# Performance work log

Hardware: AMD Instinct MI355X
Metric: run time of the kernel (lower is better)

## Reference

```python
import math
import jax, jax.numpy as jnp
import numpy as np

D_MODEL = 256
NUM_FEATURES = 512  # 2 * d_model (module default)
BATCH, SEQ = 4, 4096
EPS = 1e-6
INPUT_SCALE = 0.25  # keeps exp(xW/sqrt(d) - ||x||^2/2) numerically meaningful


def _make_projection(key):
    # Orthogonal random features: ceil(M/d)=2 QR blocks, then sqrt(|gauss|) row scaling.
    k1, k2, k3 = jax.random.split(key, 3)
    q1, _ = jnp.linalg.qr(jax.random.normal(k1, (D_MODEL, D_MODEL), jnp.float32))
    q2, _ = jnp.linalg.qr(jax.random.normal(k2, (D_MODEL, D_MODEL), jnp.float32))
    proj = jnp.concatenate([q1, q2], axis=1)[:, :NUM_FEATURES]  # (d, M)
    scaling = jnp.sqrt(jnp.abs(jax.random.normal(k3, (D_MODEL, 1), jnp.float32)))
    return proj * scaling


def setup_inputs() -> dict:
    key = jax.random.key(0)
    kq, kk, kv, kp = jax.random.split(key, 4)
    shape = (BATCH, SEQ, D_MODEL)
    return {
        "query": jax.random.normal(kq, shape, jnp.float32) * INPUT_SCALE,
        "key": jax.random.normal(kk, shape, jnp.float32) * INPUT_SCALE,
        "value": jax.random.normal(kv, shape, jnp.float32) * INPUT_SCALE,
        "projection": _make_projection(kp),  # (d_model, num_features) buffer
    }


def _phi(x, projection):
    # phi(x) = exp(xW/sqrt(d) - ||x||^2/2) / sqrt(M)
    d = x.shape[-1]
    m = projection.shape[-1]
    proj = jnp.matmul(x, projection) / math.sqrt(d)  # (B, L, M)
    sq = 0.5 * jnp.sum(x * x, axis=-1, keepdims=True)  # (B, L, 1)
    return jnp.exp(proj - sq) / math.sqrt(m)


def reference(query, key, value, projection):
    qp = _phi(query, projection)  # (B, L, M)
    kp = _phi(key, projection)    # (B, L, M)
    B, L, M = qp.shape
    D = value.shape[-1]

    # Causal linear attention: running KV-state scan, O(B*M*D) state
    # (same math as cumsum of k' (outer) v, without materializing (B,L,M,D)).
    def step(carry, inp):
        kv_state, k_state = carry  # (B,M,D), (B,M)
        q_t, k_t, v_t = inp        # (B,M), (B,M), (B,D)
        kv_state = kv_state + k_t[:, :, None] * v_t[:, None, :]
        k_state = k_state + k_t
        num = jnp.einsum('bm,bmd->bd', q_t, kv_state)
        den = jnp.einsum('bm,bm->b', q_t, k_state)[:, None] + EPS
        return (kv_state, k_state), num / den

    init = (jnp.zeros((B, M, D), qp.dtype), jnp.zeros((B, M), qp.dtype))
    xs = (jnp.swapaxes(qp, 0, 1), jnp.swapaxes(kp, 0, 1), jnp.swapaxes(value, 0, 1))
    _, out = jax.lax.scan(step, init, xs)  # (L, B, D)
    return jnp.swapaxes(out, 0, 1)  # (B, L, D)
```

## Files before the change

### kernel.cpp

```cpp
#include <hip/hip_runtime.h>

#define B_ 4
#define L_ 4096
#define D_ 256
#define M_ 512
#define C_ 256
#define NC_ 16
#define NG_ (B_*NC_)
#define EPS_ 1e-6f
#define RSQRT_D_ 0.0625f
#define RSQRT_M_ 0.044194173824159216f

typedef __attribute__((ext_vector_type(8))) short short8;
typedef __attribute__((ext_vector_type(4))) short short4v;
typedef __attribute__((ext_vector_type(4))) float floatx4;

__device__ __forceinline__ short f2b(float f) {
  union { float f; unsigned u; } c; c.f = f;
  unsigned r = c.u + 0x7fffu + ((c.u >> 16) & 1u);
  return (short)(r >> 16);
}
__device__ __forceinline__ float b2f(short s) {
  union { unsigned u; float f; } c; c.u = ((unsigned)(unsigned short)s) << 16;
  return c.f;
}

#define OFF_SB   0u
#define OFF_WT   16777216u
#define OFF_QP   17039360u
#define OFF_KP   33816576u
#define OFF_KPT  50593792u
#define OFF_VT   67371008u
#define OFF_AM   75759616u
#define OFF_PB   84148224u
#define OFF_ZP   100925440u

__device__ __forceinline__ void mfma_tile_gemm(
    const short* __restrict__ Ag, int lda,
    const short* __restrict__ Bg, int ldb,
    int K, short* sA, short* sB, floatx4 acc[4][4])
{
  const int tid  = threadIdx.x;
  const int lane = tid & 63;
  const int wave = tid >> 6;
  const int wm = wave >> 1, wn = wave & 1;
  const int q = lane >> 4, ml = lane & 15;

  short8 pa[4], pb[4];
  #pragma unroll
  for (int it = 0; it < 4; ++it) {
    int ci = tid + 256 * it;
    int m = ci >> 3, k8 = ci & 7;
    pa[it] = *(const short8*)(Ag + (size_t)m * lda + k8 * 8);
    pb[it] = *(const short8*)(Bg + (size_t)m * ldb + k8 * 8);
  }
  for (int k0 = 0; k0 < K; k0 += 64) {
    #pragma unroll
    for (int it = 0; it < 4; ++it) {
      int ci = tid + 256 * it;
      int m = ci >> 3, k8 = ci & 7;
      int dst = (k8 >> 2) * 512 + (m >> 4) * 64 + (k8 & 3) * 16 + ((m & 15) ^ k8);
      *(short8*)(sA + dst * 8) = pa[it];
      *(short8*)(sB + dst * 8) = pb[it];
    }
    if (k0 + 64 < K) {
      #pragma unroll
      for (int it = 0; it < 4; ++it) {
        int ci = tid + 256 * it;
        int m = ci >> 3, k8 = ci & 7;
        pa[it] = *(const short8*)(Ag + (size_t)m * lda + k0 + 64 + k8 * 8);
        pb[it] = *(const short8*)(Bg + (size_t)m * ldb + k0 + 64 + k8 * 8);
      }
    }
    __syncthreads();
    #pragma unroll
    for (int ks = 0; ks < 2; ++ks) {
      short8 a[4], b[4];
      int k8 = ks * 4 + q;
      #pragma unroll
      for (int i = 0; i < 4; ++i) {
        int ca = ks * 512 + (wm * 4 + i) * 64 + q * 16 + (ml ^ k8);
        a[i] = *(const short8*)(sA + ca * 8);
        int cb = ks * 512 + (wn * 4 + i) * 64 + q * 16 + (ml ^ k8);
        b[i] = *(const short8*)(sB + cb * 8);
      }
      #pragma unroll
      for (int i = 0; i < 4; ++i)
        #pragma unroll
        for (int j = 0; j < 4; ++j)
          acc[i][j] = __builtin_amdgcn_mfma_f32_16x16x32_bf16(a[i], b[j], acc[i][j], 0, 0, 0);
    }
    __syncthreads();
  }
}

__global__ __launch_bounds__(256) void transpose_cvt_kernel(
    const float* __restrict__ v, const float* __restrict__ W,
    short* __restrict__ vT, short* __restrict__ Wt)
{
  const int z = blockIdx.z;
  const float* src; short* dst; int ld_in, ld_out;
  if (z < NG_) {
    if (blockIdx.x >= 4) return;
    src = v + (size_t)z * (C_*D_) + (size_t)blockIdx.y * 64 * D_ + blockIdx.x * 64;
    dst = vT + (size_t)z * (D_*C_) + (size_t)blockIdx.x * 64 * C_ + blockIdx.y * 64;
    ld_in = D_; ld_out = C_;
  } else {
    src = W + (size_t)blockIdx.y * 64 * M_ + blockIdx.x * 64;
    dst = Wt + (size_t)blockIdx.x * 64 * D_ + blockIdx.y * 64;
    ld_in = M_; ld_out = D_;
  }
  __shared__ short sm[64 * 65];
  const int tid = threadIdx.x;
  #pragma unroll
  for (int it = 0; it < 4; ++it) {
    int ci = tid + 256 * it;
    int row = ci >> 4, c4 = ci & 15;
    float4 x = *(const float4*)(src + (size_t)row * ld_in + c4 * 4);
    sm[(c4 * 4 + 0) * 65 + row] = f2b(x.x);
    sm[(c4 * 4 + 1) * 65 + row] = f2b(x.y);
    sm[(c4 * 4 + 2) * 65 + row] = f2b(x.z);
    sm[(c4 * 4 + 3) * 65 + row] = f2b(x.w);
  }
  __syncthreads();
  #pragma unroll
  for (int it = 0; it < 2; ++it) {
    int ci = tid + 256 * it;
    int dr = ci >> 3, t8 = ci & 7;
    short8 o;
    #pragma unroll
    for (int u = 0; u < 8; ++u) o[u] = sm[dr * 65 + t8 * 8 + u];
    *(short8*)(dst + (size_t)dr * ld_out + t8 * 8) = o;
  }
}

__global__ __launch_bounds__(256) void phi_mfma_kernel(
    const float* __restrict__ qin, const float* __restrict__ kin,
    const short* __restrict__ Wt,
    short* __restrict__ qp, short* __restrict__ kp, short* __restrict__ kpT)
{
  const bool is_k = (blockIdx.z == 1);
  const float* X = is_k ? kin : qin;
  short* outP = is_k ? kp : qp;
  const int id = blockIdx.x + 4 * blockIdx.y;
  const int row0 = ((id & 7) + 8 * (id >> 5)) * 128;
  const int col0 = ((id >> 3) & 3) * 128;
  __shared__ short smem[17664];
  short* sA = smem;
  short* sB = smem + 8192;
  float* sqs = (float*)(smem + 17408);
  const int tid = threadIdx.x, lane = tid & 63, wave = tid >> 6;
  const int wm = wave >> 1, wn = wave & 1, q = lane >> 4, ml = lane & 15;
  floatx4 acc[4][4];
  #pragma unroll
  for (int i = 0; i < 4; ++i)
    #pragma unroll
    for (int j = 0; j < 4; ++j) acc[i][j] = (floatx4){0.f,0.f,0.f,0.f};

  float4 px0[4], px1[4];
  #pragma unroll
  for (int it = 0; it < 4; ++it) {
    int ci = tid + 256 * it;
    int m = ci >> 3, c = ci & 7;
    const float* src = X + (size_t)(row0 + m) * D_ + c * 8;
    px0[it] = *(const float4*)src;
    px1[it] = *(const float4*)(src + 4);
  }
  float ssq[4] = {0.f, 0.f, 0.f, 0.f};
  for (int k0 = 0; k0 < D_; k0 += 64) {
    #pragma unroll
    for (int it = 0; it < 4; ++it) {
      int ci = tid + 256 * it;
      int m = ci >> 3, c = ci & 7;
      short8 wb = *(const short8*)(Wt + (size_t)(col0 + m) * D_ + k0 + c * 8);
      float4 x0 = px0[it], x1 = px1[it];
      short8 vv;
      vv[0] = f2b(x0.x); vv[1] = f2b(x0.y); vv[2] = f2b(x0.z); vv[3] = f2b(x0.w);
      vv[4] = f2b(x1.x); vv[5] = f2b(x1.y); vv[6] = f2b(x1.z); vv[7] = f2b(x1.w);
      ssq[it] += x0.x*x0.x + x0.y*x0.y + x0.z*x0.z + x0.w*x0.w
               + x1.x*x1.x + x1.y*x1.y + x1.z*x1.z + x1.w*x1.w;
      *(short8*)(sA + (c * 128 + (m ^ c)) * 8) = vv;
      *(short8*)(sB + (c * 128 + (m ^ c)) * 8) = wb;
    }
    if (k0 + 64 < D_) {
      #pragma unroll
      for (int it = 0; it < 4; ++it) {
        int ci = tid + 256 * it;
        int m = ci >> 3, c = ci & 7;
        const float* src = X + (size_t)(row0 + m) * D_ + k0 + 64 + c * 8;
        px0[it] = *(const float4*)src;
        px1[it] = *(const float4*)(src + 4);
      }
    }
    __syncthreads();
    #pragma unroll
    for (int ks = 0; ks < 2; ++ks) {
      short8 a[4], b[4];
      int c = ks * 4 + q;
      #pragma unroll
      for (int i = 0; i < 4; ++i) {
        int ra = (wm * 64 + i * 16 + ml) ^ c;
        a[i] = *(const short8*)(sA + (c * 128 + ra) * 8);
        int rb = (wn * 64 + i * 16 + ml) ^ c;
        b[i] = *(const short8*)(sB + (c * 128 + rb) * 8);
      }
      #pragma unroll
      for (int i = 0; i < 4; ++i)
        #pragma unroll
        for (int j = 0; j < 4; ++j)
          acc[i][j] = __builtin_amdgcn_mfma_f32_16x16x32_bf16(a[i], b[j], acc[i][j], 0, 0, 0);
    }
    __syncthreads();
  }
  #pragma unroll
  for (int o = 1; o < 8; o <<= 1)
    #pragma unroll
    for (int it = 0; it < 4; ++it) ssq[it] += __shfl_xor(ssq[it], o);
  if ((tid & 7) == 0) {
    #pragma unroll
    for (int it = 0; it < 4; ++it) sqs[(tid >> 3) + 32 * it] = 0.5f * ssq[it];
  }
  __syncthreads();
  #pragma unroll
  for (int i = 0; i < 4; ++i) {
    int rl = wm * 64 + i * 16 + q * 4;
    float sqv[4];
    #pragma unroll
    for (int r = 0; r < 4; ++r) sqv[r] = sqs[rl + r];
    #pragma unroll
    for (int j = 0; j < 4; ++j) {
      int cl = wn * 64 + j * 16 + ml;
      short4v tb;
      #pragma unroll
      for (int r = 0; r < 4; ++r) {
        float pv = __expf(fmaf(acc[i][j][r], RSQRT_D_, -sqv[r])) * RSQRT_M_;
        short bv = f2b(pv);
        outP[(size_t)(row0 + rl + r) * M_ + col0 + cl] = bv;
        tb[r] = bv;
      }
      if (is_k)
        *(short4v*)(smem + (size_t)cl * 136 + rl) = tb;
    }
  }
  if (is_k) {
    __syncthreads();
    int g = row0 >> 8, tb0 = row0 & 255;
    #pragma unroll
    for (int it = 0; it < 8; ++it) {
      int ci = tid + 256 * it;
      int t8 = ci & 15, cc = ci >> 4;
      short8 vv = *(const short8*)(smem + (size_t)cc * 136 + t8 * 8);
      *(short8*)(kpT + (size_t)g * (M_*C_) + (size_t)(col0 + cc) * C_ + tb0 + t8 * 8) = vv;
    }
  }
}

__global__ __launch_bounds__(256) void mega_kernel(
    const short* __restrict__ vT, const short* __restrict__ kpT,
    const short* __restrict__ qp, const short* __restrict__ kp,
    short* __restrict__ Sb, short* __restrict__ Am, float* __restrict__ ZP)
{
  const int id = blockIdx.x + 4 * blockIdx.y + 16 * blockIdx.z;
  const int g  = (id & 7) + 8 * (id >> 7);
  const int inner = (id >> 3) & 15;
  const int bx = inner & 3, by = inner >> 2;
  __shared__ short smem[16384];
  const int tid = threadIdx.x;

  if (by == 3) {
    const int mb = bx & 1, p = bx >> 1;
    if (p >= 2) return;
    const int m = mb * 256 + tid;
    const short* base = kp + ((size_t)g * C_ + p * 128) * M_ + m;
    float s = 0.f;
    #pragma unroll 8
    for (int t = 0; t < 128; ++t) s += b2f(base[(size_t)t * M_]);
    ZP[((size_t)g * 2 + p) * M_ + m] = s;
    return;
  }

  floatx4 acc[4][4];
  #pragma unroll
  for (int i = 0; i < 4; ++i)
    #pragma unroll
    for (int j = 0; j < 4; ++j) acc[i][j] = (floatx4){0.f,0.f,0.f,0.f};
  const int lane = tid & 63, wave = tid >> 6;
  const int wm = wave >> 1, wn = wave & 1, q = lane >> 4, ln = lane & 15;

  if (by < 2) {
    const int m0 = bx * 128, d0 = by * 128;
    mfma_tile_gemm(vT + (size_t)g * (D_*C_) + (size_t)d0 * C_, C_,
                   kpT + (size_t)g * (M_*C_) + (size_t)m0 * C_, C_, C_,
                   smem, smem + 8192, acc);
    #pragma unroll
    for (int i = 0; i < 4; ++i) {
      int rl = d0 + wm * 64 + i * 16 + q * 4;
      #pragma unroll
      for (int j = 0; j < 4; ++j) {
        int cl = m0 + wn * 64 + j * 16 + ln;
        #pragma unroll
        for (int r = 0; r < 4; ++r)
          Sb[((size_t)g * D_ + rl + r) * M_ + cl] = f2b(acc[i][j][r]);
      }
    }
  } else {
    const int tt0 = (bx >> 1) * 128, tp0 = (bx & 1) * 128;
    short* Ag = Am + (size_t)g * (C_*C_);
    if (tp0 > tt0) {
      short8 z8 = 0;
      #pragma unroll
      for (int it = 0; it < 8; ++it) {
        int ci = tid + 256 * it;
        int row = ci >> 4, c8 = ci & 15;
        *(short8*)(Ag + (size_t)(tt0 + row) * C_ + tp0 + c8 * 8) = z8;
      }
      return;
    }
    const size_t cb = (size_t)g * C_;
    mfma_tile_gemm(qp + (cb + tt0) * M_, M_, kp + (cb + tp0) * M_, M_, M_,
                   smem, smem + 8192, acc);
    #pragma unroll
    for (int i = 0; i < 4; ++i) {
      int rl = tt0 + wm * 64 + i * 16 + q * 4;
      #pragma unroll
      for (int j = 0; j < 4; ++j) {
        int cl = tp0 + wn * 64 + j * 16 + ln;
        #pragma unroll
        for (int r = 0; r < 4; ++r) {
          short bv = (cl <= rl + r) ? f2b(acc[i][j][r]) : (short)0;
          Ag[(size_t)(rl + r) * C_ + cl] = bv;
        }
      }
    }
  }
}

__global__ __launch_bounds__(256) void prefixS_kernel(
    const short* __restrict__ Sb, short* __restrict__ Pb)
{
  int j = blockIdx.x * 256 + threadIdx.x;
  int b = j >> 17, e = j & 131071;
  float run = 0.f;
  size_t idx = ((size_t)b * NC_) * 131072 + e;
  for (int i = 0; i < NC_; ++i) {
    float t = b2f(Sb[idx]);
    Pb[idx] = f2b(run);
    run += t;
    idx += 131072;
  }
}

__global__ __launch_bounds__(256) void out_mfma_kernel(
    const short* __restrict__ qp, const short* __restrict__ Pb,
    const short* __restrict__ Am, const short* __restrict__ vT,
    const float* __restrict__ ZP, float* __restrict__ out)
{
  const int id = blockIdx.x + 2 * blockIdx.y + 4 * blockIdx.z;
  const int g  = (id & 7) + 8 * (id >> 5);
  const int inner = (id >> 3) & 3;
  const int d0 = (inner & 1) * 128, tt0 = (inner >> 1) * 128;
  __shared__ short smem[16384];
  __shared__ float zbuf[512];
  __shared__ float dbuf[128];
  short* sA = smem; short* sB = smem + 8192;
  const int tid = threadIdx.x, lane = tid & 63, wave = tid >> 6;
  const int wm = wave >> 1, wn = wave & 1, q = lane >> 4, ml = lane & 15;
  const int r8 = tid >> 3;

  {
    int b = g >> 4, gi = g & 15;
    float s0 = 0.f, s1 = 0.f;
    const float* zp0 = ZP + (size_t)(b * NC_) * 2 * M_;
    for (int i = 0; i < gi; ++i) {
      const float* r = zp0 + (size_t)i * 2 * M_;
      s0 += r[tid] + r[M_ + tid];
      s1 += r[tid + 256] + r[M_ + tid + 256];
    }
    zbuf[tid] = s0; zbuf[tid + 256] = s1;
    if (tid < 128) dbuf[tid] = 0.f;
  }
  __syncthreads();

  floatx4 acc[4][4];
  #pragma unroll
  for (int i = 0; i < 4; ++i)
    #pragma unroll
    for (int j = 0; j < 4; ++j) acc[i][j] = (floatx4){0.f,0.f,0.f,0.f};

  {
    const short* Ag = qp + ((size_t)g * C_ + tt0) * M_;
    const short* Bg = Pb + (size_t)g * (D_*M_) + (size_t)d0 * M_;
    float dp[4] = {0.f, 0.f, 0.f, 0.f};
    short8 pa[4], pb[4];
    #pragma unroll
    for (int it = 0; it < 4; ++it) {
      int ci = tid + 256 * it;
      int m = ci >> 3, k8 = ci & 7;
      pa[it] = *(const short8*)(Ag + (size_t)m * M_ + k8 * 8);
      pb[it] = *(const short8*)(Bg + (size_t)m * M_ + k8 * 8);
    }
    for (int k0 = 0; k0 < M_; k0 += 64) {
      #pragma unroll
      for (int it = 0; it < 4; ++it) {
        int ci = tid + 256 * it;
        int m = ci >> 3, k8 = ci & 7;
        int dst = (k8 >> 2) * 512 + (m >> 4) * 64 + (k8 & 3) * 16 + ((m & 15) ^ k8);
        *(short8*)(sA + dst * 8) = pa[it];
        *(short8*)(sB + dst * 8) = pb[it];
        const float* zz = zbuf + k0 + k8 * 8;
        float d = 0.f;
        #pragma unroll
        for (int u = 0; u < 8; ++u) d = fmaf(b2f(pa[it][u]), zz[u], d);
        dp[it] += d;
      }
      if (k0 + 64 < M_) {
        #pragma unroll
        for (int it = 0; it < 4; ++it) {
          int ci = tid + 256 * it;
          int m = ci >> 3, k8 = ci & 7;
          pa[it] = *(const short8*)(Ag + (size_t)m * M_ + k0 + 64 + k8 * 8);
          pb[it] = *(const short8*)(Bg + (size_t)m * M_ + k0 + 64 + k8 * 8);
        }
      }
      __syncthreads();
      #pragma unroll
      for (int ks = 0; ks < 2; ++ks) {
        short8 a[4], b[4];
        int k8 = ks * 4 + q;
        #pragma unroll
        for (int i = 0; i < 4; ++i) {
          int ca = ks * 512 + (wm * 4 + i) * 64 + q * 16 + (ml ^ k8);
          a[i] = *(const short8*)(sA + ca * 8);
          int cb = ks * 512 + (wn * 4 + i) * 64 + q * 16 + (ml ^ k8);
          b[i] = *(const short8*)(sB + cb * 8);
        }
        #pragma unroll
        for (int i = 0; i < 4; ++i)
          #pragma unroll
          for (int j = 0; j < 4; ++j)
            acc[i][j] = __builtin_amdgcn_mfma_f32_16x16x32_bf16(a[i], b[j], acc[i][j], 0, 0, 0);
      }
      __syncthreads();
    }
    #pragma unroll
    for (int o = 1; o < 8; o <<= 1)
      #pragma unroll
      for (int it = 0; it < 4; ++it) dp[it] += __shfl_xor(dp[it], o);
    if ((tid & 7) == 0) {
      #pragma unroll
      for (int it = 0; it < 4; ++it) dbuf[r8 + 32 * it] += dp[it];
    }
  }

  {
    const short* Ag = Am + ((size_t)g * C_ + tt0) * C_;
    const short* Bg = vT + (size_t)g * (D_*C_) + (size_t)d0 * C_;
    float dp[4] = {0.f, 0.f, 0.f, 0.f};
    short8 pa[4], pb[4];
    #pragma unroll
    for (int it = 0; it < 4; ++it) {
      int ci = tid + 256 * it;
      int m = ci >> 3, k8 = ci & 7;
      pa[it] = *(const short8*)(Ag + (size_t)m * C_ + k8 * 8);
      pb[it] = *(const short8*)(Bg + (size_t)m * C_ + k8 * 8);
    }
    for (int k0 = 0; k0 < C_; k0 += 64) {
      #pragma unroll
      for (int it = 0; it < 4; ++it) {
        int ci = tid + 256 * it;
        int m = ci >> 3, k8 = ci & 7;
        int dst = (k8 >> 2) * 512 + (m >> 4) * 64 + (k8 & 3) * 16 + ((m & 15) ^ k8);
        *(short8*)(sA + dst * 8) = pa[it];
        *(short8*)(sB + dst * 8) = pb[it];
        float d = 0.f;
        #pragma unroll
        for (int u = 0; u < 8; ++u) d += b2f(pa[it][u]);
        dp[it] += d;
      }
      if (k0 + 64 < C_) {
        #pragma unroll
        for (int it = 0; it < 4; ++it) {
          int ci = tid + 256 * it;
          int m = ci >> 3, k8 = ci & 7;
          pa[it] = *(const short8*)(Ag + (size_t)m * C_ + k0 + 64 + k8 * 8);
          pb[it] = *(const short8*)(Bg + (size_t)m * C_ + k0 + 64 + k8 * 8);
        }
      }
      __syncthreads();
      #pragma unroll
      for (int ks = 0; ks < 2; ++ks) {
        short8 a[4], b[4];
        int k8 = ks * 4 + q;
        #pragma unroll
        for (int i = 0; i < 4; ++i) {
          int ca = ks * 512 + (wm * 4 + i) * 64 + q * 16 + (ml ^ k8);
          a[i] = *(const short8*)(sA + ca * 8);
          int cb = ks * 512 + (wn * 4 + i) * 64 + q * 16 + (ml ^ k8);
          b[i] = *(const short8*)(sB + cb * 8);
        }
        #pragma unroll
        for (int i = 0; i < 4; ++i)
          #pragma unroll
          for (int j = 0; j < 4; ++j)
            acc[i][j] = __builtin_amdgcn_mfma_f32_16x16x32_bf16(a[i], b[j], acc[i][j], 0, 0, 0);
      }
      __syncthreads();
    }
    #pragma unroll
    for (int o = 1; o < 8; o <<= 1)
      #pragma unroll
      for (int it = 0; it < 4; ++it) dp[it] += __shfl_xor(dp[it], o);
    if ((tid & 7) == 0) {
      #pragma unroll
      for (int it = 0; it < 4; ++it) dbuf[r8 + 32 * it] += dp[it];
    }
  }
  __syncthreads();

  #pragma unroll
  for (int i = 0; i < 4; ++i) {
    int lr = wm * 64 + i * 16 + q * 4;
    #pragma unroll
    for (int r = 0; r < 4; ++r) {
      int grow = g * C_ + tt0 + lr + r;
      float rc = 1.0f / (dbuf[lr + r] + EPS_);
      #pragma unroll
      for (int j = 0; j < 4; ++j) {
        int cl = d0 + wn * 64 + j * 16 + ml;
        out[(size_t)grow * D_ + cl] = acc[i][j][r] * rc;
      }
    }
  }
}

extern "C" void kernel_launch(void* const* d_in, const int* in_sizes, int n_in,
                              void* d_out, int out_size, void* d_ws, size_t ws_size,
                              hipStream_t stream) {
  const float* q = (const float*)d_in[0];
  const float* k = (const float*)d_in[1];
  const float* v = (const float*)d_in[2];
  const float* W = (const float*)d_in[3];
  float* out = (float*)d_out;
  char* ws = (char*)d_ws;

  short* Sb  = (short*)(ws + OFF_SB);
  short* Wt  = (short*)(ws + OFF_WT);
  short* qp  = (short*)(ws + OFF_QP);
  short* kp  = (short*)(ws + OFF_KP);
  short* kpT = (short*)(ws + OFF_KPT);
  short* vT  = (short*)(ws + OFF_VT);
  short* Am  = (short*)(ws + OFF_AM);
  short* Pb  = (short*)(ws + OFF_PB);
  float* ZP  = (float*)(ws + OFF_ZP);

  transpose_cvt_kernel<<<dim3(8, 4, NG_ + 1), 256, 0, stream>>>(v, W, vT, Wt);
  phi_mfma_kernel<<<dim3(M_/128, (B_*L_)/128, 2), 256, 0, stream>>>(q, k, Wt, qp, kp, kpT);
  mega_kernel<<<dim3(4, 4, NG_), 256, 0, stream>>>(vT, kpT, qp, kp, Sb, Am, ZP);
  prefixS_kernel<<<(B_*D_*M_)/256, 256, 0, stream>>>(Sb, Pb);
  out_mfma_kernel<<<dim3(D_/128, C_/128, NG_), 256, 0, stream>>>(qp, Pb, Am, vT, ZP, out);
}
```

Before: 161.7 us.

## Fuse key column sums into phi, vectorize prefix scan, halve output tile rows

The per-chunk key feature sums (ZP) are now computed in the phi kernel epilogue from the bf16 values it just produced. This removes the strided column-sum blocks from mega_kernel, which now launches 12 tiles per group instead of 16. The prefix scan over chunk states loads and stores 8 bf16 values per thread with all chunks held in registers, cutting its thread count by eight. The output kernel's row tile shrinks from 128 to 64, doubling its block count for better occupancy at the cost of re-reading the B operand more often.

```diff
diff --git a/kernel.cpp b/kernel.cpp
--- a/kernel.cpp
+++ b/kernel.cpp
@@ -137,7 +137,8 @@
 __global__ __launch_bounds__(256) void phi_mfma_kernel(
     const float* __restrict__ qin, const float* __restrict__ kin,
     const short* __restrict__ Wt,
-    short* __restrict__ qp, short* __restrict__ kp, short* __restrict__ kpT)
+    short* __restrict__ qp, short* __restrict__ kp, short* __restrict__ kpT,
+    float* __restrict__ ZP)
 {
   const bool is_k = (blockIdx.z == 1);
   const float* X = is_k ? kin : qin;
@@ -146,6 +147,7 @@
   const int row0 = ((id & 7) + 8 * (id >> 5)) * 128;
   const int col0 = ((id >> 3) & 3) * 128;
   __shared__ short smem[17664];
+  __shared__ float zsb[256];
   short* sA = smem;
   short* sB = smem + 8192;
   float* sqs = (float*)(smem + 17408);
@@ -221,6 +223,7 @@
     for (int it = 0; it < 4; ++it) sqs[(tid >> 3) + 32 * it] = 0.5f * ssq[it];
   }
   __syncthreads();
+  float csum[4] = {0.f, 0.f, 0.f, 0.f};
   #pragma unroll
   for (int i = 0; i < 4; ++i) {
     int rl = wm * 64 + i * 16 + q * 4;
@@ -237,12 +240,23 @@
         short bv = f2b(pv);
         outP[(size_t)(row0 + rl + r) * M_ + col0 + cl] = bv;
         tb[r] = bv;
+        if (is_k) csum[j] += b2f(bv);
       }
       if (is_k)
         *(short4v*)(smem + (size_t)cl * 136 + rl) = tb;
     }
   }
   if (is_k) {
+    #pragma unroll
+    for (int j = 0; j < 4; ++j) {
+      csum[j] += __shfl_xor(csum[j], 16);
+      csum[j] += __shfl_xor(csum[j], 32);
+    }
+    if (lane < 16) {
+      #pragma unroll
+      for (int j = 0; j < 4; ++j)
+        zsb[wm * 128 + wn * 64 + j * 16 + ml] = csum[j];
+    }
     __syncthreads();
     int g = row0 >> 8, tb0 = row0 & 255;
     #pragma unroll
@@ -252,32 +266,26 @@
       short8 vv = *(const short8*)(smem + (size_t)cc * 136 + t8 * 8);
       *(short8*)(kpT + (size_t)g * (M_*C_) + (size_t)(col0 + cc) * C_ + tb0 + t8 * 8) = vv;
     }
+    if (tid < 128) {
+      float s = zsb[tid] + zsb[128 + tid];
+      int p = (row0 >> 7) & 1;
+      ZP[((size_t)g * 2 + p) * M_ + col0 + tid] = s;
+    }
   }
 }
 
 __global__ __launch_bounds__(256) void mega_kernel(
     const short* __restrict__ vT, const short* __restrict__ kpT,
     const short* __restrict__ qp, const short* __restrict__ kp,
-    short* __restrict__ Sb, short* __restrict__ Am, float* __restrict__ ZP)
+    short* __restrict__ Sb, short* __restrict__ Am)
 {
-  const int id = blockIdx.x + 4 * blockIdx.y + 16 * blockIdx.z;
-  const int g  = (id & 7) + 8 * (id >> 7);
-  const int inner = (id >> 3) & 15;
+  const int id = blockIdx.x + 4 * blockIdx.y + 12 * blockIdx.z;
+  const int t12 = id >> 3;
+  const int g  = (id & 7) + 8 * (t12 / 12);
+  const int inner = t12 % 12;
   const int bx = inner & 3, by = inner >> 2;
   __shared__ short smem[16384];
   const int tid = threadIdx.x;
-
-  if (by == 3) {
-    const int mb = bx & 1, p = bx >> 1;
-    if (p >= 2) return;
-    const int m = mb * 256 + tid;
-    const short* base = kp + ((size_t)g * C_ + p * 128) * M_ + m;
-    float s = 0.f;
-    #pragma unroll 8
-    for (int t = 0; t < 128; ++t) s += b2f(base[(size_t)t * M_]);
-    ZP[((size_t)g * 2 + p) * M_ + m] = s;
-    return;
-  }
 
   floatx4 acc[4][4];
   #pragma unroll
@@ -339,14 +347,19 @@
     const short* __restrict__ Sb, short* __restrict__ Pb)
 {
   int j = blockIdx.x * 256 + threadIdx.x;
-  int b = j >> 17, e = j & 131071;
-  float run = 0.f;
-  size_t idx = ((size_t)b * NC_) * 131072 + e;
+  int b = j >> 14, e8 = j & 16383;
+  size_t base = ((size_t)b * NC_) * 131072 + (size_t)e8 * 8;
+  short8 t[NC_];
+  #pragma unroll
+  for (int i = 0; i < NC_; ++i)
+    t[i] = *(const short8*)(Sb + base + (size_t)i * 131072);
+  float run[8] = {0.f,0.f,0.f,0.f,0.f,0.f,0.f,0.f};
+  #pragma unroll
   for (int i = 0; i < NC_; ++i) {
-    float t = b2f(Sb[idx]);
-    Pb[idx] = f2b(run);
-    run += t;
-    idx += 131072;
+    short8 o;
+    #pragma unroll
+    for (int u = 0; u < 8; ++u) { o[u] = f2b(run[u]); run[u] += b2f(t[i][u]); }
+    *(short8*)(Pb + base + (size_t)i * 131072) = o;
   }
 }
 
@@ -355,14 +368,14 @@
     const short* __restrict__ Am, const short* __restrict__ vT,
     const float* __restrict__ ZP, float* __restrict__ out)
 {
-  const int id = blockIdx.x + 2 * blockIdx.y + 4 * blockIdx.z;
-  const int g  = (id & 7) + 8 * (id >> 5);
-  const int inner = (id >> 3) & 3;
-  const int d0 = (inner & 1) * 128, tt0 = (inner >> 1) * 128;
-  __shared__ short smem[16384];
+  const int id = blockIdx.x + 2 * blockIdx.y + 8 * blockIdx.z;
+  const int g  = (id & 7) + 8 * (id >> 6);
+  const int inner = (id >> 3) & 7;
+  const int d0 = (inner & 1) * 128, tt0 = (inner >> 1) * 64;
+  __shared__ short smem[12288];
   __shared__ float zbuf[512];
-  __shared__ float dbuf[128];
-  short* sA = smem; short* sB = smem + 8192;
+  __shared__ float dbuf[64];
+  short* sA = smem; short* sB = smem + 4096;
   const int tid = threadIdx.x, lane = tid & 63, wave = tid >> 6;
   const int wm = wave >> 1, wn = wave & 1, q = lane >> 4, ml = lane & 15;
   const int r8 = tid >> 3;
@@ -377,65 +390,84 @@
       s1 += r[tid + 256] + r[M_ + tid + 256];
     }
     zbuf[tid] = s0; zbuf[tid + 256] = s1;
-    if (tid < 128) dbuf[tid] = 0.f;
+    if (tid < 64) dbuf[tid] = 0.f;
   }
   __syncthreads();
 
-  floatx4 acc[4][4];
-  #pragma unroll
-  for (int i = 0; i < 4; ++i)
+  floatx4 acc[2][4];
+  #pragma unroll
+  for (int i = 0; i < 2; ++i)
     #pragma unroll
     for (int j = 0; j < 4; ++j) acc[i][j] = (floatx4){0.f,0.f,0.f,0.f};
 
   {
     const short* Ag = qp + ((size_t)g * C_ + tt0) * M_;
     const short* Bg = Pb + (size_t)g * (D_*M_) + (size_t)d0 * M_;
-    float dp[4] = {0.f, 0.f, 0.f, 0.f};
-    short8 pa[4], pb[4];
+    float dp[2] = {0.f, 0.f};
+    short8 pa[2], pb[4];
+    #pragma unroll
+    for (int it = 0; it < 2; ++it) {
+      int ci = tid + 256 * it;
+      int m = ci >> 3, k8 = ci & 7;
+      pa[it] = *(const short8*)(Ag + (size_t)m * M_ + k8 * 8);
+    }
     #pragma unroll
     for (int it = 0; it < 4; ++it) {
       int ci = tid + 256 * it;
       int m = ci >> 3, k8 = ci & 7;
-      pa[it] = *(const short8*)(Ag + (size_t)m * M_ + k8 * 8);
       pb[it] = *(const short8*)(Bg + (size_t)m * M_ + k8 * 8);
     }
     for (int k0 = 0; k0 < M_; k0 += 64) {
+      #pragma unroll
+      for (int it = 0; it < 2; ++it) {
+        int ci = tid + 256 * it;
+        int m = ci >> 3, k8 = ci & 7;
+        int dst = (k8 >> 2) * 256 + (m >> 4) * 64 + (k8 & 3) * 16 + ((m & 15) ^ k8);
+        *(short8*)(sA + dst * 8) = pa[it];
+        const float* zz = zbuf + k0 + k8 * 8;
+        float d = 0.f;
+        #pragma unroll
+        for (int u = 0; u < 8; ++u) d = fmaf(b2f(pa[it][u]), zz[u], d);
+        dp[it] += d;
+      }
       #pragma unroll
       for (int it = 0; it < 4; ++it) {
         int ci = tid + 256 * it;
         int m = ci >> 3, k8 = ci & 7;
         int dst = (k8 >> 2) * 512 + (m >> 4) * 64 + (k8 & 3) * 16 + ((m & 15) ^ k8);
-        *(short8*)(sA + dst * 8) = pa[it];
         *(short8*)(sB + dst * 8) = pb[it];
-        const float* zz = zbuf + k0 + k8 * 8;
-        float d = 0.f;
-        #pragma unroll
-        for (int u = 0; u < 8; ++u) d = fmaf(b2f(pa[it][u]), zz[u], d);
-        dp[it] += d;
       }
       if (k0 + 64 < M_) {
+        #pragma unroll
+        for (int it = 0; it < 2; ++it) {
+          int ci = tid + 256 * it;
+          int m = ci >> 3, k8 = ci & 7;
+          pa[it] = *(const short8*)(Ag + (size_t)m * M_ + k0 + 64 + k8 * 8);
+        }
         #pragma unroll
         for (int it = 0; it < 4; ++it) {
           int ci = tid + 256 * it;
           int m = ci >> 3, k8 = ci & 7;
-          pa[it] = *(const short8*)(Ag + (size_t)m * M_ + k0 + 64 + k8 * 8);
           pb[it] = *(const short8*)(Bg + (size_t)m * M_ + k0 + 64 + k8 * 8);
         }
       }
       __syncthreads();
       #pragma unroll
       for (int ks = 0; ks < 2; ++ks) {
-        short8 a[4], b[4];
+        short8 a[2], b[4];
         int k8 = ks * 4 + q;
         #pragma unroll
-        for (int i = 0; i < 4; ++i) {
-          int ca = ks * 512 + (wm * 4 + i) * 64 + q * 16 + (ml ^ k8);
+        for (int i = 0; i < 2; ++i) {
+          int ca = ks * 256 + (wm * 2 + i) * 64 + q * 16 + (ml ^ k8);
           a[i] = *(const short8*)(sA + ca * 8);
-          int cb = ks * 512 + (wn * 4 + i) * 64 + q * 16 + (ml ^ k8);
-          b[i] = *(const short8*)(sB + cb * 8);
-        }
-        #pragma unroll
-        for (int i = 0; i < 4; ++i)
+        }
+        #pragma unroll
+        for (int j = 0; j < 4; ++j) {
+          int cb = ks * 512 + (wn * 4 + j) * 64 + q * 16 + (ml ^ k8);
+          b[j] = *(const short8*)(sB + cb * 8);
+        }
+        #pragma unroll
+        for (int i = 0; i < 2; ++i)
           #pragma unroll
           for (int j = 0; j < 4; ++j)
             acc[i][j] = __builtin_amdgcn_mfma_f32_16x16x32_bf16(a[i], b[j], acc[i][j], 0, 0, 0);
@@ -445,61 +477,80 @@
     #pragma unroll
     for (int o = 1; o < 8; o <<= 1)
       #pragma unroll
-      for (int it = 0; it < 4; ++it) dp[it] += __shfl_xor(dp[it], o);
+      for (int it = 0; it < 2; ++it) dp[it] += __shfl_xor(dp[it], o);
     if ((tid & 7) == 0) {
       #pragma unroll
-      for (int it = 0; it < 4; ++it) dbuf[r8 + 32 * it] += dp[it];
+      for (int it = 0; it < 2; ++it) dbuf[r8 + 32 * it] += dp[it];
     }
   }
 
   {
     const short* Ag = Am + ((size_t)g * C_ + tt0) * C_;
     const short* Bg = vT + (size_t)g * (D_*C_) + (size_t)d0 * C_;
-    float dp[4] = {0.f, 0.f, 0.f, 0.f};
-    short8 pa[4], pb[4];
+    float dp[2] = {0.f, 0.f};
+    short8 pa[2], pb[4];
+    #pragma unroll
+    for (int it = 0; it < 2; ++it) {
+      int ci = tid + 256 * it;
+      int m = ci >> 3, k8 = ci & 7;
+      pa[it] = *(const short8*)(Ag + (size_t)m * C_ + k8 * 8);
+    }
     #pragma unroll
     for (int it = 0; it < 4; ++it) {
       int ci = tid + 256 * it;
       int m = ci >> 3, k8 = ci & 7;
-      pa[it] = *(const short8*)(Ag + (size_t)m * C_ + k8 * 8);
       pb[it] = *(const short8*)(Bg + (size_t)m * C_ + k8 * 8);
     }
     for (int k0 = 0; k0 < C_; k0 += 64) {
+      #pragma unroll
+      for (int it = 0; it < 2; ++it) {
+        int ci = tid + 256 * it;
+        int m = ci >> 3, k8 = ci & 7;
+        int dst = (k8 >> 2) * 256 + (m >> 4) * 64 + (k8 & 3) * 16 + ((m & 15) ^ k8);
+        *(short8*)(sA + dst * 8) = pa[it];
+        float d = 0.f;
+        #pragma unroll
+        for (int u = 0; u < 8; ++u) d += b2f(pa[it][u]);
+        dp[it] += d;
+      }
       #pragma unroll
       for (int it = 0; it < 4; ++it) {
         int ci = tid + 256 * it;
         int m = ci >> 3, k8 = ci & 7;
         int dst = (k8 >> 2) * 512 + (m >> 4) * 64 + (k8 & 3) * 16 + ((m & 15) ^ k8);
-        *(short8*)(sA + dst * 8) = pa[it];
         *(short8*)(sB + dst * 8) = pb[it];
-        float d = 0.f;
-        #pragma unroll
-        for (int u = 0; u < 8; ++u) d += b2f(pa[it][u]);
-        dp[it] += d;
       }
       if (k0 + 64 < C_) {
+        #pragma unroll
+        for (int it = 0; it < 2; ++it) {
+          int ci = tid + 256 * it;
+          int m = ci >> 3, k8 = ci & 7;
+          pa[it] = *(const short8*)(Ag + (size_t)m * C_ + k0 + 64 + k8 * 8);
+        }
         #pragma unroll
         for (int it = 0; it < 4; ++it) {
           int ci = tid + 256 * it;
           int m = ci >> 3, k8 = ci & 7;
-          pa[it] = *(const short8*)(Ag + (size_t)m * C_ + k0 + 64 + k8 * 8);
           pb[it] = *(const short8*)(Bg + (size_t)m * C_ + k0 + 64 + k8 * 8);
         }
       }
       __syncthreads();
       #pragma unroll
       for (int ks = 0; ks < 2; ++ks) {
-        short8 a[4], b[4];
+        short8 a[2], b[4];
         int k8 = ks * 4 + q;
         #pragma unroll
-        for (int i = 0; i < 4; ++i) {
-          int ca = ks * 512 + (wm * 4 + i) * 64 + q * 16 + (ml ^ k8);
+        for (int i = 0; i < 2; ++i) {
+          int ca = ks * 256 + (wm * 2 + i) * 64 + q * 16 + (ml ^ k8);
           a[i] = *(const short8*)(sA + ca * 8);
-          int cb = ks * 512 + (wn * 4 + i) * 64 + q * 16 + (ml ^ k8);
-          b[i] = *(const short8*)(sB + cb * 8);
-        }
-        #pragma unroll
-        for (int i = 0; i < 4; ++i)
+        }
+        #pragma unroll
+        for (int j = 0; j < 4; ++j) {
+          int cb = ks * 512 + (wn * 4 + j) * 64 + q * 16 + (ml ^ k8);
+          b[j] = *(const short8*)(sB + cb * 8);
+        }
+        #pragma unroll
+        for (int i = 0; i < 2; ++i)
           #pragma unroll
           for (int j = 0; j < 4; ++j)
             acc[i][j] = __builtin_amdgcn_mfma_f32_16x16x32_bf16(a[i], b[j], acc[i][j], 0, 0, 0);
@@ -509,17 +560,17 @@
     #pragma unroll
     for (int o = 1; o < 8; o <<= 1)
       #pragma unroll
-      for (int it = 0; it < 4; ++it) dp[it] += __shfl_xor(dp[it], o);
+      for (int it = 0; it < 2; ++it) dp[it] += __shfl_xor(dp[it], o);
     if ((tid & 7) == 0) {
       #pragma unroll
-      for (int it = 0; it < 4; ++it) dbuf[r8 + 32 * it] += dp[it];
+      for (int it = 0; it < 2; ++it) dbuf[r8 + 32 * it] += dp[it];
     }
   }
   __syncthreads();
 
   #pragma unroll
-  for (int i = 0; i < 4; ++i) {
-    int lr = wm * 64 + i * 16 + q * 4;
+  for (int i = 0; i < 2; ++i) {
+    int lr = wm * 32 + i * 16 + q * 4;
     #pragma unroll
     for (int r = 0; r < 4; ++r) {
       int grow = g * C_ + tt0 + lr + r;
@@ -554,8 +605,8 @@
   float* ZP  = (float*)(ws + OFF_ZP);
 
   transpose_cvt_kernel<<<dim3(8, 4, NG_ + 1), 256, 0, stream>>>(v, W, vT, Wt);
-  phi_mfma_kernel<<<dim3(M_/128, (B_*L_)/128, 2), 256, 0, stream>>>(q, k, Wt, qp, kp, kpT);
-  mega_kernel<<<dim3(4, 4, NG_), 256, 0, stream>>>(vT, kpT, qp, kp, Sb, Am, ZP);
-  prefixS_kernel<<<(B_*D_*M_)/256, 256, 0, stream>>>(Sb, Pb);
-  out_mfma_kernel<<<dim3(D_/128, C_/128, NG_), 256, 0, stream>>>(qp, Pb, Am, vT, ZP, out);
-}
+  phi_mfma_kernel<<<dim3(M_/128, (B_*L_)/128, 2), 256, 0, stream>>>(q, k, Wt, qp, kp, kpT, ZP);
+  mega_kernel<<<dim3(4, 3, NG_), 256, 0, stream>>>(vT, kpT, qp, kp, Sb, Am);
+  prefixS_kernel<<<(B_*D_*M_)/2048, 256, 0, stream>>>(Sb, Pb);
+  out_mfma_kernel<<<dim3(2, 4, NG_), 256, 0, stream>>>(qp, Pb, Am, vT, ZP, out);
+}
```

After: 160.6 us. No clear change (-0.7%).
